# Performance work log

Hardware: AMD Instinct MI355X
Metric: run time of the kernel (lower is better)

Reference implementation:

```python
import jax, jax.numpy as jnp
import numpy as np

TAU = 2.0
EPS = 1e-5
SG_ALPHA = 4.0  # spikingjelly default Sigmoid surrogate alpha


@jax.custom_vjp
def heaviside(x):
    return (x >= 0.0).astype(x.dtype)

def _heaviside_fwd(x):
    return heaviside(x), x

def _heaviside_bwd(x, g):
    s = jax.nn.sigmoid(SG_ALPHA * x)
    return (g * SG_ALPHA * s * (1.0 - s),)

heaviside.defvjp(_heaviside_fwd, _heaviside_bwd)


def lif(x_seq, v_th):
    """Multi-step LIF, hard reset to 0, detach_reset=True. x_seq: (T, ...)."""
    def step(v, x_t):
        v = v + (x_t - v) / TAU
        s = heaviside(v - v_th)
        v = v * (1.0 - jax.lax.stop_gradient(s))  # detached hard reset
        return v, s
    _, spikes = jax.lax.scan(step, jnp.zeros_like(x_seq[0]), x_seq)
    return spikes


def bn(y, gamma, beta, mean, var):
    # y: (T, B, C, N); inference-mode BatchNorm1d over channel dim
    inv = gamma / jnp.sqrt(var + EPS)
    return y * inv[None, None, :, None] + (beta - mean * inv)[None, None, :, None]


def setup_inputs() -> dict:
    key = jax.random.key(0)
    ks = jax.random.split(key, 8)
    T, B, C, H, W = 4, 32, 256, 32, 32
    d = {
        "x": jax.random.normal(ks[0], (T, B, C, H, W), jnp.float32),
        "q_w": jax.random.normal(ks[1], (C, C), jnp.float32) * (1.0 / np.sqrt(C)),
        "q_gamma": jnp.ones((C,), jnp.float32),
        "q_beta": jnp.zeros((C,), jnp.float32),
        "q_mean": jnp.zeros((C,), jnp.float32),
        "q_var": jnp.ones((C,), jnp.float32),
        "k_w": jax.random.normal(ks[2], (C, C), jnp.float32) * (1.0 / np.sqrt(C)),
        "k_gamma": jnp.ones((C,), jnp.float32),
        "k_beta": jnp.zeros((C,), jnp.float32),
        "k_mean": jnp.zeros((C,), jnp.float32),
        "k_var": jnp.ones((C,), jnp.float32),
        "p_w": jax.random.normal(ks[3], (C, C), jnp.float32) * (1.0 / np.sqrt(C)),
        "p_b": jnp.zeros((C,), jnp.float32),
        "p_gamma": jnp.ones((C,), jnp.float32),
        "p_beta": jnp.zeros((C,), jnp.float32),
        "p_mean": jnp.zeros((C,), jnp.float32),
        "p_var": jnp.ones((C,), jnp.float32),
    }
    return d


def reference(x, q_w, q_gamma, q_beta, q_mean, q_var,
              k_w, k_gamma, k_beta, k_mean, k_var,
              p_w, p_b, p_gamma, p_beta, p_mean, p_var):
    T, B, C, H, W = x.shape
    num_heads = 8
    dh = C // num_heads
    N = H * W
    xs = x.reshape(T, B, C, N)

    # Q branch: 1x1 conv (C x C matmul) -> BN -> LIF
    q = bn(jnp.einsum('oc,tbcn->tbon', q_w, xs), q_gamma, q_beta, q_mean, q_var)
    q_spikes = lif(q, 1.0)                                # (T,B,C,N)
    q_h = q_spikes.reshape(T, B, num_heads, dh, N)

    # K branch
    k = bn(jnp.einsum('oc,tbcn->tbon', k_w, xs), k_gamma, k_beta, k_mean, k_var)
    k_spikes = lif(k, 1.0)
    k_h = k_spikes.reshape(T, B, num_heads, dh, N)

    # channel-sum pooled Q per head -> attn LIF (v_th=0.5) -> elementwise mult with K
    q_sum = jnp.sum(q_h, axis=3, keepdims=True)           # (T,B,h,1,N)
    attn = lif(q_sum, 0.5)
    x_one = attn * k_h                                    # (T,B,h,dh,N)

    # projection: 1x1 conv with bias -> BN -> LIF
    xo = x_one.reshape(T, B, C, N)
    xo = jnp.einsum('oc,tbcn->tbon', p_w, xo) + p_b[None, None, :, None]
    xo = bn(xo, p_gamma, p_beta, p_mean, p_var).reshape(T, B, C, H, W)
    x_final = lif(xo, 1.0)
    return x_final
```

## Files before the change

kernel.cpp:

```cpp
#include <hip/hip_runtime.h>
#include <cstdint>
#include <cstddef>

#define T_DIM 4
#define B_DIM 32
#define C_DIM 256
#define N_DIM 1024
#define NHEAD 8
#define DHEAD 32
#define NWRD 32

__device__ __forceinline__ float lif_step(float& v, float x, float vth) {
    v = __fadd_rn(v, __fmul_rn(__fsub_rn(x, v), 0.5f));
    const float s = (v >= vth) ? 1.0f : 0.0f;
    if (s != 0.0f) v = 0.0f;
    return s;
}

__device__ __forceinline__ void async_copy16(const float* g, float* l) {
    __builtin_amdgcn_global_load_lds(
        (const __attribute__((address_space(1))) unsigned int*)g,
        (__attribute__((address_space(3))) unsigned int*)l, 16, 0, 0);
}

#define FMA_ROW(r, av)                                \
    acc[(r)*8+0] = fmaf(av, b0.x, acc[(r)*8+0]);      \
    acc[(r)*8+1] = fmaf(av, b0.y, acc[(r)*8+1]);      \
    acc[(r)*8+2] = fmaf(av, b0.z, acc[(r)*8+2]);      \
    acc[(r)*8+3] = fmaf(av, b0.w, acc[(r)*8+3]);      \
    acc[(r)*8+4] = fmaf(av, b1.x, acc[(r)*8+4]);      \
    acc[(r)*8+5] = fmaf(av, b1.y, acc[(r)*8+5]);      \
    acc[(r)*8+6] = fmaf(av, b1.z, acc[(r)*8+6]);      \
    acc[(r)*8+7] = fmaf(av, b1.w, acc[(r)*8+7]);

#define FMA_8x8()        \
    FMA_ROW(0, a0.x)     \
    FMA_ROW(1, a0.y)     \
    FMA_ROW(2, a0.z)     \
    FMA_ROW(3, a0.w)     \
    FMA_ROW(4, a1.x)     \
    FMA_ROW(5, a1.y)     \
    FMA_ROW(6, a1.z)     \
    FMA_ROW(7, a1.w)

__global__ __launch_bounds__(256) void k_transpose(
    const float* __restrict__ qw, const float* __restrict__ kw,
    const float* __restrict__ pw, float* __restrict__ wqk_t,
    float* __restrict__ p_t)
{
    const int i = blockIdx.x * 256 + threadIdx.x;
    if (i < C_DIM * 512) {
        const int k = i >> 9, col = i & 511;
        const int h = col >> 6, j = col & 63;
        wqk_t[i] = (j < 32) ? qw[(size_t)(h * 32 + j) * C_DIM + k]
                            : kw[(size_t)(h * 32 + j - 32) * C_DIM + k];
    } else {
        const int i2 = i - C_DIM * 512;
        const int k = i2 >> 8, c = i2 & 255;
        p_t[i2] = pw[(size_t)c * C_DIM + k];
    }
}

__global__ __launch_bounds__(256, 2) void k_qk(
    const float* __restrict__ x, const float* __restrict__ wqk,
    const float* __restrict__ qg, const float* __restrict__ qbeta,
    const float* __restrict__ qmean, const float* __restrict__ qvar,
    const float* __restrict__ kg, const float* __restrict__ kbeta,
    const float* __restrict__ kmean, const float* __restrict__ kvar,
    uint32_t* __restrict__ xbits)
{
    __shared__ float w_lds[2][32 * 128];
    __shared__ float x_lds[2][32 * 128];
    __shared__ float inv_lds[128];
    __shared__ float bias_lds[128];
    __shared__ float    qsum_lds[256];
    __shared__ float    attn_lds[256];
    __shared__ uint32_t pack_lds[256];

    const int tid = threadIdx.x;
    const int hp = blockIdx.x, nt = blockIdx.y, b = blockIdx.z;
    const int n0g = nt * 128;

    const int  mg   = tid >> 4;
    const int  m0   = mg << 3;
    const int  ng   = tid & 15;
    const int  n0   = ng << 2;
    const int  hsel = mg >> 3;
    const bool is_q = ((mg & 7) < 4);

    if (tid < 128) {
        const int m = tid;
        const int hs = m >> 6, j = m & 63;
        const int h = hp * 2 + hs;
        const bool q = (j < 32);
        const float* g  = q ? qg    : kg;
        const float* be = q ? qbeta : kbeta;
        const float* me = q ? qmean : kmean;
        const float* va = q ? qvar  : kvar;
        const int ch = h * DHEAD + (q ? j : j - 32);
        const float iv = __fdiv_rn(g[ch], __fsqrt_rn(__fadd_rn(va[ch], 1e-5f)));
        inv_lds[m]  = iv;
        bias_lds[m] = __fsub_rn(be[ch], __fmul_rn(me[ch], iv));
    }

    const int skl  = tid >> 5;
    const int scol = (tid & 31) << 2;
    const float* wgp = wqk + (size_t)skl * 512 + hp * 128 + scol;

    float vstate[64];
    #pragma unroll
    for (int i = 0; i < 64; i++) vstate[i] = 0.0f;
    float v_attn = 0.0f;

    {
        const float* xgp = x + ((size_t)b * C_DIM + skl) * N_DIM + n0g + scol;
        #pragma unroll
        for (int r = 0; r < 4; r++) {
            async_copy16(wgp + (size_t)(r * 8) * 512,  &w_lds[0][r * 1024 + tid * 4]);
            async_copy16(xgp + (size_t)(r * 8) * N_DIM, &x_lds[0][r * 1024 + tid * 4]);
        }
    }

    float acc[64];
    #pragma unroll
    for (int i = 0; i < 64; i++) acc[i] = 0.0f;

    for (int g = 0; g < 32; ++g) {
        const int cur = g & 1;
        __syncthreads();
        if (g + 1 < 32) {
            const int g1 = g + 1, tt = g1 >> 3, kk = (g1 & 7) * 32;
            const float* xgp = x + ((size_t)(tt * B_DIM + b) * C_DIM + kk + skl) * N_DIM
                               + n0g + scol;
            float* wd = &w_lds[1 - cur][0];
            float* xd = &x_lds[1 - cur][0];
            #pragma unroll
            for (int r = 0; r < 4; r++) {
                async_copy16(wgp + (size_t)(kk + r * 8) * 512,  wd + r * 1024 + tid * 4);
                async_copy16(xgp + (size_t)(r * 8) * N_DIM,     xd + r * 1024 + tid * 4);
            }
        }
        {
            const float* wl = &w_lds[cur][0];
            const float* xl = &x_lds[cur][0];
            #pragma unroll 2
            for (int k = 0; k < 32; k++) {
                const float4 a0 = *(const float4*)(wl + k * 128 + m0);
                const float4 a1 = *(const float4*)(wl + k * 128 + m0 + 4);
                const float4 b0 = *(const float4*)(xl + k * 128 + n0);
                const float4 b1 = *(const float4*)(xl + k * 128 + 64 + n0);
                FMA_8x8()
            }
        }

        if ((g & 7) == 7) {
            const int t = g >> 3;
            #pragma unroll
            for (int r = 0; r < 8; r++) {
                const float iv = inv_lds[m0 + r];
                const float bs = bias_lds[m0 + r];
                #pragma unroll
                for (int j = 0; j < 8; j++) {
                    const float y = __fadd_rn(__fmul_rn(acc[r * 8 + j], iv), bs);
                    acc[r * 8 + j] = lif_step(vstate[r * 8 + j], y, 1.0f);
                }
            }
            qsum_lds[tid] = 0.0f;
            pack_lds[tid] = 0u;
            __syncthreads();
            if (is_q) {
                #pragma unroll
                for (int j = 0; j < 8; j++) {
                    const int col = (j < 4) ? (n0 + j) : (64 + n0 + (j - 4));
                    float cs = acc[j];
                    #pragma unroll
                    for (int r = 1; r < 8; r++) cs += acc[r * 8 + j];
                    atomicAdd(&qsum_lds[hsel * 128 + col], cs);
                }
            }
            __syncthreads();
            attn_lds[tid] = lif_step(v_attn, qsum_lds[tid], 0.5f);
            __syncthreads();
            if (!is_q) {
                #pragma unroll
                for (int r = 0; r < 8; r++) {
                    const int krow = ((mg & 7) - 4) * 8 + r;
                    #pragma unroll
                    for (int ci = 0; ci < 2; ci++) {
                        uint32_t nib = 0;
                        #pragma unroll
                        for (int jj = 0; jj < 4; jj++) {
                            const int col = ci * 64 + n0 + jj;
                            if (acc[r * 8 + ci * 4 + jj] != 0.0f &&
                                attn_lds[hsel * 128 + col] != 0.0f)
                                nib |= (1u << jj);
                        }
                        if (nib) {
                            const int word = ci * 2 + (ng >> 3);
                            const int shf  = (ng & 7) * 4;
                            atomicOr(&pack_lds[hsel * 128 + krow * 4 + word], nib << shf);
                        }
                    }
                }
            }
            __syncthreads();
            {
                const int hs2  = tid >> 7;
                const int rem  = tid & 127;
                const int krow = rem >> 2, word = rem & 3;
                const int ch = (hp * 2 + hs2) * DHEAD + krow;
                xbits[((size_t)(t * B_DIM + b) * C_DIM + ch) * NWRD + nt * 4 + word]
                    = pack_lds[tid];
            }
            #pragma unroll
            for (int i = 0; i < 64; i++) acc[i] = 0.0f;
        }
    }
}

__global__ __launch_bounds__(256, 2) void k_proj(
    const uint32_t* __restrict__ xbits, const float* __restrict__ pt,
    const float* __restrict__ pbias, const float* __restrict__ pg,
    const float* __restrict__ pbeta, const float* __restrict__ pmean,
    const float* __restrict__ pvar, float* __restrict__ out)
{
    __shared__ float w_lds[2][32 * 128];
    __shared__ float x_lds[2][32 * 128];
    __shared__ float inv_lds[128];
    __shared__ float bias_lds[128];
    __shared__ float pb_lds[128];

    const int tid = threadIdx.x;
    const int mt = blockIdx.x, nt = blockIdx.y, b = blockIdx.z;
    const int n0g = nt * 128;
    const int c0  = mt * 128;

    const int mg = tid >> 4, m0 = mg << 3;
    const int ng = tid & 15, n0 = ng << 2;

    if (tid < 128) {
        const int ch = c0 + tid;
        const float iv = __fdiv_rn(pg[ch], __fsqrt_rn(__fadd_rn(pvar[ch], 1e-5f)));
        inv_lds[tid]  = iv;
        bias_lds[tid] = __fsub_rn(pbeta[ch], __fmul_rn(pmean[ch], iv));
        pb_lds[tid]   = pbias[ch];
    }

    const int skl  = tid >> 5;
    const int scol = (tid & 31) << 2;
    const float* wgp = pt + (size_t)skl * 256 + c0 + scol;

    const int urow = tid >> 3, cg = tid & 7;
    const int wsel = nt * 4 + (cg >> 1);
    const int ushf = (cg & 1) * 16;

    float vstate[64];
    #pragma unroll
    for (int i = 0; i < 64; i++) vstate[i] = 0.0f;

    #define BITS_AT(G) xbits[((size_t)((G) >> 3) * B_DIM + b) * C_DIM * NWRD \
                             + (size_t)(((G) & 7) * 32 + urow) * NWRD + wsel]

    {
        const uint32_t u0 = BITS_AT(0);
        const uint32_t bits = (u0 >> ushf) & 0xffffu;
        float* xw = &x_lds[0][tid * 16];
        #pragma unroll
        for (int q4 = 0; q4 < 4; q4++) {
            float4 f;
            f.x = ((bits >> (q4 * 4 + 0)) & 1u) ? 1.0f : 0.0f;
            f.y = ((bits >> (q4 * 4 + 1)) & 1u) ? 1.0f : 0.0f;
            f.z = ((bits >> (q4 * 4 + 2)) & 1u) ? 1.0f : 0.0f;
            f.w = ((bits >> (q4 * 4 + 3)) & 1u) ? 1.0f : 0.0f;
            *(float4*)(xw + q4 * 4) = f;
        }
        #pragma unroll
        for (int r = 0; r < 4; r++)
            async_copy16(wgp + (size_t)(r * 8) * 256, &w_lds[0][r * 1024 + tid * 4]);
    }
    uint32_t u_a = BITS_AT(1);

    float acc[64];
    #pragma unroll
    for (int i = 0; i < 64; i++) acc[i] = 0.0f;

    for (int g = 0; g < 32; ++g) {
        const int cur = g & 1;
        __syncthreads();
        if (g + 1 < 32) {
            const int kk = ((g + 1) & 7) * 32;
            const uint32_t bits = (u_a >> ushf) & 0xffffu;
            float* xw = &x_lds[1 - cur][tid * 16];
            #pragma unroll
            for (int q4 = 0; q4 < 4; q4++) {
                float4 f;
                f.x = ((bits >> (q4 * 4 + 0)) & 1u) ? 1.0f : 0.0f;
                f.y = ((bits >> (q4 * 4 + 1)) & 1u) ? 1.0f : 0.0f;
                f.z = ((bits >> (q4 * 4 + 2)) & 1u) ? 1.0f : 0.0f;
                f.w = ((bits >> (q4 * 4 + 3)) & 1u) ? 1.0f : 0.0f;
                *(float4*)(xw + q4 * 4) = f;
            }
            float* wd = &w_lds[1 - cur][0];
            #pragma unroll
            for (int r = 0; r < 4; r++)
                async_copy16(wgp + (size_t)(kk + r * 8) * 256, wd + r * 1024 + tid * 4);
        }
        if (g + 2 < 32) u_a = BITS_AT(g + 2);
        {
            const float* wl = &w_lds[cur][0];
            const float* xl = &x_lds[cur][0];
            #pragma unroll 2
            for (int k = 0; k < 32; k++) {
                const float4 a0 = *(const float4*)(wl + k * 128 + m0);
                const float4 a1 = *(const float4*)(wl + k * 128 + m0 + 4);
                const float4 b0 = *(const float4*)(xl + k * 128 + n0);
                const float4 b1 = *(const float4*)(xl + k * 128 + 64 + n0);
                FMA_8x8()
            }
        }

        if ((g & 7) == 7) {
            const int t = g >> 3;
            #pragma unroll
            for (int r = 0; r < 8; r++) {
                const int ch = c0 + m0 + r;
                const float iv = inv_lds[m0 + r];
                const float bs = bias_lds[m0 + r];
                const float pb = pb_lds[m0 + r];
                float* ob = out + ((size_t)(t * B_DIM + b) * C_DIM + ch) * N_DIM + n0g;
                float oAv[4], oBv[4];
                #pragma unroll
                for (int j = 0; j < 8; j++) {
                    float y = __fadd_rn(acc[r * 8 + j], pb);
                    y = __fadd_rn(__fmul_rn(y, iv), bs);
                    const float s = lif_step(vstate[r * 8 + j], y, 1.0f);
                    if (j < 4) oAv[j] = s; else oBv[j - 4] = s;
                }
                float4 oA, oB;
                oA.x = oAv[0]; oA.y = oAv[1]; oA.z = oAv[2]; oA.w = oAv[3];
                oB.x = oBv[0]; oB.y = oBv[1]; oB.z = oBv[2]; oB.w = oBv[3];
                *(float4*)(ob + n0)      = oA;
                *(float4*)(ob + 64 + n0) = oB;
            }
            #pragma unroll
            for (int i = 0; i < 64; i++) acc[i] = 0.0f;
        }
    }
    #undef BITS_AT
}

extern "C" void kernel_launch(void* const* d_in, const int* in_sizes, int n_in,
                              void* d_out, int out_size, void* d_ws, size_t ws_size,
                              hipStream_t stream) {
    const float* x    = (const float*)d_in[0];
    const float* q_w  = (const float*)d_in[1];
    const float* q_g  = (const float*)d_in[2];
    const float* q_b  = (const float*)d_in[3];
    const float* q_m  = (const float*)d_in[4];
    const float* q_v  = (const float*)d_in[5];
    const float* k_w  = (const float*)d_in[6];
    const float* k_g  = (const float*)d_in[7];
    const float* k_b  = (const float*)d_in[8];
    const float* k_m  = (const float*)d_in[9];
    const float* k_v  = (const float*)d_in[10];
    const float* p_w  = (const float*)d_in[11];
    const float* p_b  = (const float*)d_in[12];
    const float* p_g  = (const float*)d_in[13];
    const float* p_be = (const float*)d_in[14];
    const float* p_m  = (const float*)d_in[15];
    const float* p_v  = (const float*)d_in[16];

    float*    wqk_t = (float*)d_ws;
    float*    p_t   = (float*)((char*)d_ws + 524288);
    uint32_t* xbits = (uint32_t*)((char*)d_ws + 786432);
    float*    out   = (float*)d_out;

    k_transpose<<<768, 256, 0, stream>>>(q_w, k_w, p_w, wqk_t, p_t);

    dim3 g1(NHEAD / 2, N_DIM / 128, B_DIM);
    k_qk<<<g1, 256, 0, stream>>>(x, wqk_t, q_g, q_b, q_m, q_v,
                                 k_g, k_b, k_m, k_v, xbits);

    dim3 g2(C_DIM / 128, N_DIM / 128, B_DIM);
    k_proj<<<g2, 256, 0, stream>>>(xbits, p_t, p_b, p_g, p_be, p_m, p_v, out);
}
```

Measured before the change: 832.5 us.

## Read weights via scalar loads, shrink tiles, ballot-pack spikes per wavefront

Both GEMM kernels stop staging weights in LDS. Each wavefront now owns 16 output rows, and the weights arrive through inline-asm s_load_dwordx16 scalar loads that are broadcast to all lanes, while each lane handles two columns. Per-block tiles shrink to 64 rows, register accumulators drop from 64 to 32, and launch bounds rise to 4 blocks per CU to raise occupancy. In k_qk, the LDS atomics used for the Q-sum and spike packing are replaced by a two-wave partial-sum exchange and __ballot bit packing. The trade-offs are less register-level reuse per thread, an s_waitcnt after every k-pair that stalls each scalar load, and reliance on the scalar cache for weight bandwidth.

```diff
diff --git a/kernel.cpp b/kernel.cpp
--- a/kernel.cpp
+++ b/kernel.cpp
@@ -10,6 +10,8 @@
 #define DHEAD 32
 #define NWRD 32
 
+typedef float f32x16 __attribute__((ext_vector_type(16)));
+
 __device__ __forceinline__ float lif_step(float& v, float x, float vth) {
     v = __fadd_rn(v, __fmul_rn(__fsub_rn(x, v), 0.5f));
     const float s = (v >= vth) ? 1.0f : 0.0f;
@@ -23,25 +25,33 @@
         (__attribute__((address_space(3))) unsigned int*)l, 16, 0, 0);
 }
 
-#define FMA_ROW(r, av)                                \
-    acc[(r)*8+0] = fmaf(av, b0.x, acc[(r)*8+0]);      \
-    acc[(r)*8+1] = fmaf(av, b0.y, acc[(r)*8+1]);      \
-    acc[(r)*8+2] = fmaf(av, b0.z, acc[(r)*8+2]);      \
-    acc[(r)*8+3] = fmaf(av, b0.w, acc[(r)*8+3]);      \
-    acc[(r)*8+4] = fmaf(av, b1.x, acc[(r)*8+4]);      \
-    acc[(r)*8+5] = fmaf(av, b1.y, acc[(r)*8+5]);      \
-    acc[(r)*8+6] = fmaf(av, b1.z, acc[(r)*8+6]);      \
-    acc[(r)*8+7] = fmaf(av, b1.w, acc[(r)*8+7]);
-
-#define FMA_8x8()        \
-    FMA_ROW(0, a0.x)     \
-    FMA_ROW(1, a0.y)     \
-    FMA_ROW(2, a0.z)     \
-    FMA_ROW(3, a0.w)     \
-    FMA_ROW(4, a1.x)     \
-    FMA_ROW(5, a1.y)     \
-    FMA_ROW(6, a1.z)     \
-    FMA_ROW(7, a1.w)
+#define KSTEP2(KK, WST) { \
+    f32x16 A0, A1; \
+    asm volatile("s_load_dwordx16 %0, %2, %3\n\t" \
+                 "s_load_dwordx16 %1, %2, %4\n\t" \
+                 "s_waitcnt lgkmcnt(0)" \
+                 : "=&s"(A0), "=&s"(A1) \
+                 : "s"(wb), "n"((KK) * (WST)), "n"(((KK) + 1) * (WST))); \
+    const float b0A = xl[(KK) * 128 + l]; \
+    const float b0B = xl[(KK) * 128 + 64 + l]; \
+    const float b1A = xl[(KK) * 128 + 128 + l]; \
+    const float b1B = xl[(KK) * 128 + 192 + l]; \
+    _Pragma("unroll") \
+    for (int r_ = 0; r_ < 16; ++r_) { \
+        acc[r_ * 2]     = fmaf(A0[r_], b0A, acc[r_ * 2]); \
+        acc[r_ * 2 + 1] = fmaf(A0[r_], b0B, acc[r_ * 2 + 1]); \
+    } \
+    _Pragma("unroll") \
+    for (int r_ = 0; r_ < 16; ++r_) { \
+        acc[r_ * 2]     = fmaf(A1[r_], b1A, acc[r_ * 2]); \
+        acc[r_ * 2 + 1] = fmaf(A1[r_], b1B, acc[r_ * 2 + 1]); \
+    } }
+
+#define KLOOP(WST) \
+    KSTEP2(0, WST)  KSTEP2(2, WST)  KSTEP2(4, WST)  KSTEP2(6, WST) \
+    KSTEP2(8, WST)  KSTEP2(10, WST) KSTEP2(12, WST) KSTEP2(14, WST) \
+    KSTEP2(16, WST) KSTEP2(18, WST) KSTEP2(20, WST) KSTEP2(22, WST) \
+    KSTEP2(24, WST) KSTEP2(26, WST) KSTEP2(28, WST) KSTEP2(30, WST)
 
 __global__ __launch_bounds__(256) void k_transpose(
     const float* __restrict__ qw, const float* __restrict__ kw,
@@ -61,7 +71,7 @@
     }
 }
 
-__global__ __launch_bounds__(256, 2) void k_qk(
+__global__ __launch_bounds__(256, 4) void k_qk(
     const float* __restrict__ x, const float* __restrict__ wqk,
     const float* __restrict__ qg, const float* __restrict__ qbeta,
     const float* __restrict__ qmean, const float* __restrict__ qvar,
@@ -69,176 +79,134 @@
     const float* __restrict__ kmean, const float* __restrict__ kvar,
     uint32_t* __restrict__ xbits)
 {
-    __shared__ float w_lds[2][32 * 128];
     __shared__ float x_lds[2][32 * 128];
-    __shared__ float inv_lds[128];
-    __shared__ float bias_lds[128];
-    __shared__ float    qsum_lds[256];
-    __shared__ float    attn_lds[256];
-    __shared__ uint32_t pack_lds[256];
+    __shared__ float inv_lds[64];
+    __shared__ float bias_lds[64];
+    __shared__ float qpart_lds[2][128];
 
     const int tid = threadIdx.x;
-    const int hp = blockIdx.x, nt = blockIdx.y, b = blockIdx.z;
+    const int nt = blockIdx.x, b = blockIdx.y, h = blockIdx.z;
     const int n0g = nt * 128;
-
-    const int  mg   = tid >> 4;
-    const int  m0   = mg << 3;
-    const int  ng   = tid & 15;
-    const int  n0   = ng << 2;
-    const int  hsel = mg >> 3;
-    const bool is_q = ((mg & 7) < 4);
-
-    if (tid < 128) {
-        const int m = tid;
-        const int hs = m >> 6, j = m & 63;
-        const int h = hp * 2 + hs;
+    const int l   = tid & 63;
+    const int sw  = __builtin_amdgcn_readfirstlane(tid >> 6);
+    const bool is_q = (sw < 2);
+
+    if (tid < 64) {
+        const int j = tid;
         const bool q = (j < 32);
-        const float* g  = q ? qg    : kg;
+        const float* gp = q ? qg    : kg;
         const float* be = q ? qbeta : kbeta;
         const float* me = q ? qmean : kmean;
         const float* va = q ? qvar  : kvar;
         const int ch = h * DHEAD + (q ? j : j - 32);
-        const float iv = __fdiv_rn(g[ch], __fsqrt_rn(__fadd_rn(va[ch], 1e-5f)));
-        inv_lds[m]  = iv;
-        bias_lds[m] = __fsub_rn(be[ch], __fmul_rn(me[ch], iv));
+        const float iv = __fdiv_rn(gp[ch], __fsqrt_rn(__fadd_rn(va[ch], 1e-5f)));
+        inv_lds[j]  = iv;
+        bias_lds[j] = __fsub_rn(be[ch], __fmul_rn(me[ch], iv));
     }
 
     const int skl  = tid >> 5;
     const int scol = (tid & 31) << 2;
-    const float* wgp = wqk + (size_t)skl * 512 + hp * 128 + scol;
-
-    float vstate[64];
+
+    float vstate[32];
     #pragma unroll
-    for (int i = 0; i < 64; i++) vstate[i] = 0.0f;
-    float v_attn = 0.0f;
+    for (int i = 0; i < 32; ++i) vstate[i] = 0.0f;
+    float v_attn0 = 0.0f, v_attn1 = 0.0f;
+    float acc[32];
+    #pragma unroll
+    for (int i = 0; i < 32; ++i) acc[i] = 0.0f;
 
     {
         const float* xgp = x + ((size_t)b * C_DIM + skl) * N_DIM + n0g + scol;
         #pragma unroll
-        for (int r = 0; r < 4; r++) {
-            async_copy16(wgp + (size_t)(r * 8) * 512,  &w_lds[0][r * 1024 + tid * 4]);
+        for (int r = 0; r < 4; ++r)
             async_copy16(xgp + (size_t)(r * 8) * N_DIM, &x_lds[0][r * 1024 + tid * 4]);
-        }
-    }
-
-    float acc[64];
-    #pragma unroll
-    for (int i = 0; i < 64; i++) acc[i] = 0.0f;
-
-    for (int g = 0; g < 32; ++g) {
-        const int cur = g & 1;
+    }
+
+    const size_t woff = (size_t)h * 64 + (size_t)sw * 16;
+
+    #pragma unroll 1
+    for (int gi = 0; gi < 32; ++gi) {
+        const int cur = gi & 1;
         __syncthreads();
-        if (g + 1 < 32) {
-            const int g1 = g + 1, tt = g1 >> 3, kk = (g1 & 7) * 32;
+        if (gi + 1 < 32) {
+            const int g1 = gi + 1, tt = g1 >> 3, kk = (g1 & 7) * 32;
             const float* xgp = x + ((size_t)(tt * B_DIM + b) * C_DIM + kk + skl) * N_DIM
                                + n0g + scol;
-            float* wd = &w_lds[1 - cur][0];
             float* xd = &x_lds[1 - cur][0];
             #pragma unroll
-            for (int r = 0; r < 4; r++) {
-                async_copy16(wgp + (size_t)(kk + r * 8) * 512,  wd + r * 1024 + tid * 4);
-                async_copy16(xgp + (size_t)(r * 8) * N_DIM,     xd + r * 1024 + tid * 4);
-            }
+            for (int r = 0; r < 4; ++r)
+                async_copy16(xgp + (size_t)(r * 8) * N_DIM, xd + r * 1024 + tid * 4);
         }
         {
-            const float* wl = &w_lds[cur][0];
+            const float* wb = wqk + (size_t)((gi & 7) * 32) * 512 + woff;
             const float* xl = &x_lds[cur][0];
-            #pragma unroll 2
-            for (int k = 0; k < 32; k++) {
-                const float4 a0 = *(const float4*)(wl + k * 128 + m0);
-                const float4 a1 = *(const float4*)(wl + k * 128 + m0 + 4);
-                const float4 b0 = *(const float4*)(xl + k * 128 + n0);
-                const float4 b1 = *(const float4*)(xl + k * 128 + 64 + n0);
-                FMA_8x8()
-            }
-        }
-
-        if ((g & 7) == 7) {
-            const int t = g >> 3;
-            #pragma unroll
-            for (int r = 0; r < 8; r++) {
-                const float iv = inv_lds[m0 + r];
-                const float bs = bias_lds[m0 + r];
+            KLOOP(2048)
+        }
+
+        if ((gi & 7) == 7) {
+            const int t = gi >> 3;
+            #pragma unroll
+            for (int r = 0; r < 16; ++r) {
+                const float iv = inv_lds[sw * 16 + r];
+                const float bs = bias_lds[sw * 16 + r];
+                const float y0 = __fadd_rn(__fmul_rn(acc[r * 2],     iv), bs);
+                const float y1 = __fadd_rn(__fmul_rn(acc[r * 2 + 1], iv), bs);
+                acc[r * 2]     = lif_step(vstate[r * 2],     y0, 1.0f);
+                acc[r * 2 + 1] = lif_step(vstate[r * 2 + 1], y1, 1.0f);
+            }
+            if (is_q) {
+                float pA = acc[0], pB = acc[1];
                 #pragma unroll
-                for (int j = 0; j < 8; j++) {
-                    const float y = __fadd_rn(__fmul_rn(acc[r * 8 + j], iv), bs);
-                    acc[r * 8 + j] = lif_step(vstate[r * 8 + j], y, 1.0f);
-                }
-            }
-            qsum_lds[tid] = 0.0f;
-            pack_lds[tid] = 0u;
-            __syncthreads();
-            if (is_q) {
-                #pragma unroll
-                for (int j = 0; j < 8; j++) {
-                    const int col = (j < 4) ? (n0 + j) : (64 + n0 + (j - 4));
-                    float cs = acc[j];
-                    #pragma unroll
-                    for (int r = 1; r < 8; r++) cs += acc[r * 8 + j];
-                    atomicAdd(&qsum_lds[hsel * 128 + col], cs);
-                }
-            }
-            __syncthreads();
-            attn_lds[tid] = lif_step(v_attn, qsum_lds[tid], 0.5f);
+                for (int r = 1; r < 16; ++r) { pA += acc[r * 2]; pB += acc[r * 2 + 1]; }
+                qpart_lds[sw][l]      = pA;
+                qpart_lds[sw][64 + l] = pB;
+            }
             __syncthreads();
             if (!is_q) {
+                const float qA = qpart_lds[0][l]      + qpart_lds[1][l];
+                const float qB = qpart_lds[0][64 + l] + qpart_lds[1][64 + l];
+                const float aA = lif_step(v_attn0, qA, 0.5f);
+                const float aB = lif_step(v_attn1, qB, 0.5f);
+                uint64_t k0 = 0ull, k1 = 0ull;
                 #pragma unroll
-                for (int r = 0; r < 8; r++) {
-                    const int krow = ((mg & 7) - 4) * 8 + r;
-                    #pragma unroll
-                    for (int ci = 0; ci < 2; ci++) {
-                        uint32_t nib = 0;
-                        #pragma unroll
-                        for (int jj = 0; jj < 4; jj++) {
-                            const int col = ci * 64 + n0 + jj;
-                            if (acc[r * 8 + ci * 4 + jj] != 0.0f &&
-                                attn_lds[hsel * 128 + col] != 0.0f)
-                                nib |= (1u << jj);
-                        }
-                        if (nib) {
-                            const int word = ci * 2 + (ng >> 3);
-                            const int shf  = (ng & 7) * 4;
-                            atomicOr(&pack_lds[hsel * 128 + krow * 4 + word], nib << shf);
-                        }
-                    }
+                for (int r = 0; r < 16; ++r) {
+                    const uint64_t m0 = __ballot(acc[r * 2]     != 0.0f && aA != 0.0f);
+                    const uint64_t m1 = __ballot(acc[r * 2 + 1] != 0.0f && aB != 0.0f);
+                    if (l == r) { k0 = m0; k1 = m1; }
                 }
-            }
-            __syncthreads();
-            {
-                const int hs2  = tid >> 7;
-                const int rem  = tid & 127;
-                const int krow = rem >> 2, word = rem & 3;
-                const int ch = (hp * 2 + hs2) * DHEAD + krow;
-                xbits[((size_t)(t * B_DIM + b) * C_DIM + ch) * NWRD + nt * 4 + word]
-                    = pack_lds[tid];
-            }
-            #pragma unroll
-            for (int i = 0; i < 64; i++) acc[i] = 0.0f;
-        }
-    }
-}
-
-__global__ __launch_bounds__(256, 2) void k_proj(
+                if (l < 16) {
+                    const int ch = h * DHEAD + (sw - 2) * 16 + l;
+                    uint4 v;
+                    v.x = (uint32_t)k0; v.y = (uint32_t)(k0 >> 32);
+                    v.z = (uint32_t)k1; v.w = (uint32_t)(k1 >> 32);
+                    *(uint4*)&xbits[(((size_t)t * B_DIM + b) * C_DIM + ch) * NWRD + nt * 4] = v;
+                }
+            }
+            #pragma unroll
+            for (int i = 0; i < 32; ++i) acc[i] = 0.0f;
+        }
+    }
+}
+
+__global__ __launch_bounds__(256, 4) void k_proj(
     const uint32_t* __restrict__ xbits, const float* __restrict__ pt,
     const float* __restrict__ pbias, const float* __restrict__ pg,
     const float* __restrict__ pbeta, const float* __restrict__ pmean,
     const float* __restrict__ pvar, float* __restrict__ out)
 {
-    __shared__ float w_lds[2][32 * 128];
     __shared__ float x_lds[2][32 * 128];
-    __shared__ float inv_lds[128];
-    __shared__ float bias_lds[128];
-    __shared__ float pb_lds[128];
+    __shared__ float inv_lds[64];
+    __shared__ float bias_lds[64];
+    __shared__ float pb_lds[64];
 
     const int tid = threadIdx.x;
     const int mt = blockIdx.x, nt = blockIdx.y, b = blockIdx.z;
     const int n0g = nt * 128;
-    const int c0  = mt * 128;
-
-    const int mg = tid >> 4, m0 = mg << 3;
-    const int ng = tid & 15, n0 = ng << 2;
-
-    if (tid < 128) {
+    const int c0  = mt * 64;
+    const int l   = tid & 63;
+    const int sw  = __builtin_amdgcn_readfirstlane(tid >> 6);
+
+    if (tid < 64) {
         const int ch = c0 + tid;
         const float iv = __fdiv_rn(pg[ch], __fsqrt_rn(__fadd_rn(pvar[ch], 1e-5f)));
         inv_lds[tid]  = iv;
@@ -246,17 +214,16 @@
         pb_lds[tid]   = pbias[ch];
     }
 
-    const int skl  = tid >> 5;
-    const int scol = (tid & 31) << 2;
-    const float* wgp = pt + (size_t)skl * 256 + c0 + scol;
-
     const int urow = tid >> 3, cg = tid & 7;
     const int wsel = nt * 4 + (cg >> 1);
     const int ushf = (cg & 1) * 16;
 
-    float vstate[64];
+    float vstate[32];
     #pragma unroll
-    for (int i = 0; i < 64; i++) vstate[i] = 0.0f;
+    for (int i = 0; i < 32; ++i) vstate[i] = 0.0f;
+    float acc[32];
+    #pragma unroll
+    for (int i = 0; i < 32; ++i) acc[i] = 0.0f;
 
     #define BITS_AT(G) xbits[((size_t)((G) >> 3) * B_DIM + b) * C_DIM * NWRD \
                              + (size_t)(((G) & 7) * 32 + urow) * NWRD + wsel]
@@ -266,7 +233,7 @@
         const uint32_t bits = (u0 >> ushf) & 0xffffu;
         float* xw = &x_lds[0][tid * 16];
         #pragma unroll
-        for (int q4 = 0; q4 < 4; q4++) {
+        for (int q4 = 0; q4 < 4; ++q4) {
             float4 f;
             f.x = ((bits >> (q4 * 4 + 0)) & 1u) ? 1.0f : 0.0f;
             f.y = ((bits >> (q4 * 4 + 1)) & 1u) ? 1.0f : 0.0f;
@@ -274,25 +241,20 @@
             f.w = ((bits >> (q4 * 4 + 3)) & 1u) ? 1.0f : 0.0f;
             *(float4*)(xw + q4 * 4) = f;
         }
-        #pragma unroll
-        for (int r = 0; r < 4; r++)
-            async_copy16(wgp + (size_t)(r * 8) * 256, &w_lds[0][r * 1024 + tid * 4]);
     }
     uint32_t u_a = BITS_AT(1);
 
-    float acc[64];
-    #pragma unroll
-    for (int i = 0; i < 64; i++) acc[i] = 0.0f;
-
-    for (int g = 0; g < 32; ++g) {
-        const int cur = g & 1;
+    const size_t woff = (size_t)c0 + (size_t)sw * 16;
+
+    #pragma unroll 1
+    for (int gi = 0; gi < 32; ++gi) {
+        const int cur = gi & 1;
         __syncthreads();
-        if (g + 1 < 32) {
-            const int kk = ((g + 1) & 7) * 32;
+        if (gi + 1 < 32) {
             const uint32_t bits = (u_a >> ushf) & 0xffffu;
             float* xw = &x_lds[1 - cur][tid * 16];
             #pragma unroll
-            for (int q4 = 0; q4 < 4; q4++) {
+            for (int q4 = 0; q4 < 4; ++q4) {
                 float4 f;
                 f.x = ((bits >> (q4 * 4 + 0)) & 1u) ? 1.0f : 0.0f;
                 f.y = ((bits >> (q4 * 4 + 1)) & 1u) ? 1.0f : 0.0f;
@@ -300,50 +262,34 @@
                 f.w = ((bits >> (q4 * 4 + 3)) & 1u) ? 1.0f : 0.0f;
                 *(float4*)(xw + q4 * 4) = f;
             }
-            float* wd = &w_lds[1 - cur][0];
-            #pragma unroll
-            for (int r = 0; r < 4; r++)
-                async_copy16(wgp + (size_t)(kk + r * 8) * 256, wd + r * 1024 + tid * 4);
-        }
-        if (g + 2 < 32) u_a = BITS_AT(g + 2);
+        }
+        if (gi + 2 < 32) u_a = BITS_AT(gi + 2);
         {
-            const float* wl = &w_lds[cur][0];
+            const float* wb = pt + (size_t)((gi & 7) * 32) * 256 + woff;
             const float* xl = &x_lds[cur][0];
-            #pragma unroll 2
-            for (int k = 0; k < 32; k++) {
-                const float4 a0 = *(const float4*)(wl + k * 128 + m0);
-                const float4 a1 = *(const float4*)(wl + k * 128 + m0 + 4);
-                const float4 b0 = *(const float4*)(xl + k * 128 + n0);
-                const float4 b1 = *(const float4*)(xl + k * 128 + 64 + n0);
-                FMA_8x8()
-            }
-        }
-
-        if ((g & 7) == 7) {
-            const int t = g >> 3;
-            #pragma unroll
-            for (int r = 0; r < 8; r++) {
-                const int ch = c0 + m0 + r;
-                const float iv = inv_lds[m0 + r];
-                const float bs = bias_lds[m0 + r];
-                const float pb = pb_lds[m0 + r];
-                float* ob = out + ((size_t)(t * B_DIM + b) * C_DIM + ch) * N_DIM + n0g;
-                float oAv[4], oBv[4];
-                #pragma unroll
-                for (int j = 0; j < 8; j++) {
-                    float y = __fadd_rn(acc[r * 8 + j], pb);
-                    y = __fadd_rn(__fmul_rn(y, iv), bs);
-                    const float s = lif_step(vstate[r * 8 + j], y, 1.0f);
-                    if (j < 4) oAv[j] = s; else oBv[j - 4] = s;
-                }
-                float4 oA, oB;
-                oA.x = oAv[0]; oA.y = oAv[1]; oA.z = oAv[2]; oA.w = oAv[3];
-                oB.x = oBv[0]; oB.y = oBv[1]; oB.z = oBv[2]; oB.w = oBv[3];
-                *(float4*)(ob + n0)      = oA;
-                *(float4*)(ob + 64 + n0) = oB;
-            }
-            #pragma unroll
-            for (int i = 0; i < 64; i++) acc[i] = 0.0f;
+            KLOOP(1024)
+        }
+
+        if ((gi & 7) == 7) {
+            const int t = gi >> 3;
+            #pragma unroll
+            for (int r = 0; r < 16; ++r) {
+                const int m = sw * 16 + r;
+                const float iv = inv_lds[m];
+                const float bs = bias_lds[m];
+                const float pb = pb_lds[m];
+                float y0 = __fadd_rn(acc[r * 2],     pb);
+                float y1 = __fadd_rn(acc[r * 2 + 1], pb);
+                y0 = __fadd_rn(__fmul_rn(y0, iv), bs);
+                y1 = __fadd_rn(__fmul_rn(y1, iv), bs);
+                const float s0 = lif_step(vstate[r * 2],     y0, 1.0f);
+                const float s1 = lif_step(vstate[r * 2 + 1], y1, 1.0f);
+                float* ob = out + (((size_t)t * B_DIM + b) * C_DIM + c0 + m) * N_DIM + n0g;
+                ob[l]      = s0;
+                ob[64 + l] = s1;
+            }
+            #pragma unroll
+            for (int i = 0; i < 32; ++i) acc[i] = 0.0f;
         }
     }
     #undef BITS_AT
@@ -377,10 +323,10 @@
 
     k_transpose<<<768, 256, 0, stream>>>(q_w, k_w, p_w, wqk_t, p_t);
 
-    dim3 g1(NHEAD / 2, N_DIM / 128, B_DIM);
+    dim3 g1(N_DIM / 128, B_DIM, NHEAD);
     k_qk<<<g1, 256, 0, stream>>>(x, wqk_t, q_g, q_b, q_m, q_v,
                                  k_g, k_b, k_m, k_v, xbits);
 
-    dim3 g2(C_DIM / 128, N_DIM / 128, B_DIM);
+    dim3 g2(C_DIM / 64, N_DIM / 128, B_DIM);
     k_proj<<<g2, 256, 0, stream>>>(xbits, p_t, p_b, p_g, p_be, p_m, p_v, out);
 }
```

Result: slower. 2.850 ms (+242.4%).

## Read GEMM weights directly from global memory instead of staging in LDS

Applied to the files above, without the earlier changes.

Both the QK and projection GEMM kernels stop double-buffering the weight tile in shared memory. Inside the inner k-loop each thread now loads its 8 weight values straight from global memory (or cache) as float4. This halves the LDS footprint and removes the weight async copies, and k_qk's launch bounds are raised to allow 4 blocks per CU. The cost is global or L2 latency inside the FMA loop with no prefetch, plus register pressure from 64 accumulators and 64 state values under the tighter occupancy target.

```diff
diff --git a/kernel.cpp b/kernel.cpp
--- a/kernel.cpp
+++ b/kernel.cpp
@@ -61,7 +61,7 @@
     }
 }
 
-__global__ __launch_bounds__(256, 2) void k_qk(
+__global__ __launch_bounds__(256, 4) void k_qk(
     const float* __restrict__ x, const float* __restrict__ wqk,
     const float* __restrict__ qg, const float* __restrict__ qbeta,
     const float* __restrict__ qmean, const float* __restrict__ qvar,
@@ -69,7 +69,6 @@
     const float* __restrict__ kmean, const float* __restrict__ kvar,
     uint32_t* __restrict__ xbits)
 {
-    __shared__ float w_lds[2][32 * 128];
     __shared__ float x_lds[2][32 * 128];
     __shared__ float inv_lds[128];
     __shared__ float bias_lds[128];
@@ -105,7 +104,6 @@
 
     const int skl  = tid >> 5;
     const int scol = (tid & 31) << 2;
-    const float* wgp = wqk + (size_t)skl * 512 + hp * 128 + scol;
 
     float vstate[64];
     #pragma unroll
@@ -115,10 +113,8 @@
     {
         const float* xgp = x + ((size_t)b * C_DIM + skl) * N_DIM + n0g + scol;
         #pragma unroll
-        for (int r = 0; r < 4; r++) {
-            async_copy16(wgp + (size_t)(r * 8) * 512,  &w_lds[0][r * 1024 + tid * 4]);
+        for (int r = 0; r < 4; r++)
             async_copy16(xgp + (size_t)(r * 8) * N_DIM, &x_lds[0][r * 1024 + tid * 4]);
-        }
     }
 
     float acc[64];
@@ -132,21 +128,18 @@
             const int g1 = g + 1, tt = g1 >> 3, kk = (g1 & 7) * 32;
             const float* xgp = x + ((size_t)(tt * B_DIM + b) * C_DIM + kk + skl) * N_DIM
                                + n0g + scol;
-            float* wd = &w_lds[1 - cur][0];
             float* xd = &x_lds[1 - cur][0];
             #pragma unroll
-            for (int r = 0; r < 4; r++) {
-                async_copy16(wgp + (size_t)(kk + r * 8) * 512,  wd + r * 1024 + tid * 4);
-                async_copy16(xgp + (size_t)(r * 8) * N_DIM,     xd + r * 1024 + tid * 4);
-            }
+            for (int r = 0; r < 4; r++)
+                async_copy16(xgp + (size_t)(r * 8) * N_DIM, xd + r * 1024 + tid * 4);
         }
         {
-            const float* wl = &w_lds[cur][0];
+            const float* wg = wqk + (size_t)((g & 7) * 32) * 512 + hp * 128 + m0;
             const float* xl = &x_lds[cur][0];
             #pragma unroll 2
             for (int k = 0; k < 32; k++) {
-                const float4 a0 = *(const float4*)(wl + k * 128 + m0);
-                const float4 a1 = *(const float4*)(wl + k * 128 + m0 + 4);
+                const float4 a0 = *(const float4*)(wg + (size_t)k * 512);
+                const float4 a1 = *(const float4*)(wg + (size_t)k * 512 + 4);
                 const float4 b0 = *(const float4*)(xl + k * 128 + n0);
                 const float4 b1 = *(const float4*)(xl + k * 128 + 64 + n0);
                 FMA_8x8()
@@ -224,7 +217,6 @@
     const float* __restrict__ pbeta, const float* __restrict__ pmean,
     const float* __restrict__ pvar, float* __restrict__ out)
 {
-    __shared__ float w_lds[2][32 * 128];
     __shared__ float x_lds[2][32 * 128];
     __shared__ float inv_lds[128];
     __shared__ float bias_lds[128];
@@ -245,10 +237,6 @@
         bias_lds[tid] = __fsub_rn(pbeta[ch], __fmul_rn(pmean[ch], iv));
         pb_lds[tid]   = pbias[ch];
     }
-
-    const int skl  = tid >> 5;
-    const int scol = (tid & 31) << 2;
-    const float* wgp = pt + (size_t)skl * 256 + c0 + scol;
 
     const int urow = tid >> 3, cg = tid & 7;
     const int wsel = nt * 4 + (cg >> 1);
@@ -274,9 +262,6 @@
             f.w = ((bits >> (q4 * 4 + 3)) & 1u) ? 1.0f : 0.0f;
             *(float4*)(xw + q4 * 4) = f;
         }
-        #pragma unroll
-        for (int r = 0; r < 4; r++)
-            async_copy16(wgp + (size_t)(r * 8) * 256, &w_lds[0][r * 1024 + tid * 4]);
     }
     uint32_t u_a = BITS_AT(1);
 
@@ -288,7 +273,6 @@
         const int cur = g & 1;
         __syncthreads();
         if (g + 1 < 32) {
-            const int kk = ((g + 1) & 7) * 32;
             const uint32_t bits = (u_a >> ushf) & 0xffffu;
             float* xw = &x_lds[1 - cur][tid * 16];
             #pragma unroll
@@ -300,19 +284,15 @@
                 f.w = ((bits >> (q4 * 4 + 3)) & 1u) ? 1.0f : 0.0f;
                 *(float4*)(xw + q4 * 4) = f;
             }
-            float* wd = &w_lds[1 - cur][0];
-            #pragma unroll
-            for (int r = 0; r < 4; r++)
-                async_copy16(wgp + (size_t)(kk + r * 8) * 256, wd + r * 1024 + tid * 4);
         }
         if (g + 2 < 32) u_a = BITS_AT(g + 2);
         {
-            const float* wl = &w_lds[cur][0];
+            const float* wg = pt + (size_t)((g & 7) * 32) * 256 + c0 + m0;
             const float* xl = &x_lds[cur][0];
             #pragma unroll 2
             for (int k = 0; k < 32; k++) {
-                const float4 a0 = *(const float4*)(wl + k * 128 + m0);
-                const float4 a1 = *(const float4*)(wl + k * 128 + m0 + 4);
+                const float4 a0 = *(const float4*)(wg + (size_t)k * 256);
+                const float4 a1 = *(const float4*)(wg + (size_t)k * 256 + 4);
                 const float4 b0 = *(const float4*)(xl + k * 128 + n0);
                 const float4 b1 = *(const float4*)(xl + k * 128 + 64 + n0);
                 FMA_8x8()
```

Measured after the change: 995.0 us. +19.5%, slower.

## Double threads per block and halve per-thread register tile in both GEMMs

Applied to the files above, without the earlier changes.

Both the Q/K and projection kernels move from 256 to 512 threads per block, with each thread computing an 8x4 accumulator tile instead of 8x8. Loads, LIF epilogue, spike packing and bit unpacking are re-indexed to the new thread mapping. The goal is fewer registers per thread, higher occupancy and better latency hiding. The cost is lower arithmetic intensity per LDS read, more LDS traffic per FMA, and costlier block-wide barriers.

```diff
diff --git a/kernel.cpp b/kernel.cpp
--- a/kernel.cpp
+++ b/kernel.cpp
@@ -23,25 +23,21 @@
         (__attribute__((address_space(3))) unsigned int*)l, 16, 0, 0);
 }
 
-#define FMA_ROW(r, av)                                \
-    acc[(r)*8+0] = fmaf(av, b0.x, acc[(r)*8+0]);      \
-    acc[(r)*8+1] = fmaf(av, b0.y, acc[(r)*8+1]);      \
-    acc[(r)*8+2] = fmaf(av, b0.z, acc[(r)*8+2]);      \
-    acc[(r)*8+3] = fmaf(av, b0.w, acc[(r)*8+3]);      \
-    acc[(r)*8+4] = fmaf(av, b1.x, acc[(r)*8+4]);      \
-    acc[(r)*8+5] = fmaf(av, b1.y, acc[(r)*8+5]);      \
-    acc[(r)*8+6] = fmaf(av, b1.z, acc[(r)*8+6]);      \
-    acc[(r)*8+7] = fmaf(av, b1.w, acc[(r)*8+7]);
-
-#define FMA_8x8()        \
-    FMA_ROW(0, a0.x)     \
-    FMA_ROW(1, a0.y)     \
-    FMA_ROW(2, a0.z)     \
-    FMA_ROW(3, a0.w)     \
-    FMA_ROW(4, a1.x)     \
-    FMA_ROW(5, a1.y)     \
-    FMA_ROW(6, a1.z)     \
-    FMA_ROW(7, a1.w)
+#define FMA_ROW4(r, av)                               \
+    acc[(r)*4+0] = fmaf(av, b0.x, acc[(r)*4+0]);      \
+    acc[(r)*4+1] = fmaf(av, b0.y, acc[(r)*4+1]);      \
+    acc[(r)*4+2] = fmaf(av, b0.z, acc[(r)*4+2]);      \
+    acc[(r)*4+3] = fmaf(av, b0.w, acc[(r)*4+3]);
+
+#define FMA_8x4()        \
+    FMA_ROW4(0, a0.x)    \
+    FMA_ROW4(1, a0.y)    \
+    FMA_ROW4(2, a0.z)    \
+    FMA_ROW4(3, a0.w)    \
+    FMA_ROW4(4, a1.x)    \
+    FMA_ROW4(5, a1.y)    \
+    FMA_ROW4(6, a1.z)    \
+    FMA_ROW4(7, a1.w)
 
 __global__ __launch_bounds__(256) void k_transpose(
     const float* __restrict__ qw, const float* __restrict__ kw,
@@ -61,7 +57,7 @@
     }
 }
 
-__global__ __launch_bounds__(256, 2) void k_qk(
+__global__ __launch_bounds__(512, 4) void k_qk(
     const float* __restrict__ x, const float* __restrict__ wqk,
     const float* __restrict__ qg, const float* __restrict__ qbeta,
     const float* __restrict__ qmean, const float* __restrict__ qvar,
@@ -81,9 +77,9 @@
     const int hp = blockIdx.x, nt = blockIdx.y, b = blockIdx.z;
     const int n0g = nt * 128;
 
-    const int  mg   = tid >> 4;
+    const int  mg   = tid >> 5;
     const int  m0   = mg << 3;
-    const int  ng   = tid & 15;
+    const int  ng   = tid & 31;
     const int  n0   = ng << 2;
     const int  hsel = mg >> 3;
     const bool is_q = ((mg & 7) < 4);
@@ -107,23 +103,23 @@
     const int scol = (tid & 31) << 2;
     const float* wgp = wqk + (size_t)skl * 512 + hp * 128 + scol;
 
-    float vstate[64];
+    float vstate[32];
     #pragma unroll
-    for (int i = 0; i < 64; i++) vstate[i] = 0.0f;
+    for (int i = 0; i < 32; i++) vstate[i] = 0.0f;
     float v_attn = 0.0f;
 
     {
         const float* xgp = x + ((size_t)b * C_DIM + skl) * N_DIM + n0g + scol;
         #pragma unroll
-        for (int r = 0; r < 4; r++) {
-            async_copy16(wgp + (size_t)(r * 8) * 512,  &w_lds[0][r * 1024 + tid * 4]);
-            async_copy16(xgp + (size_t)(r * 8) * N_DIM, &x_lds[0][r * 1024 + tid * 4]);
-        }
-    }
-
-    float acc[64];
+        for (int r = 0; r < 2; r++) {
+            async_copy16(wgp + (size_t)(r * 16) * 512,  &w_lds[0][r * 2048 + tid * 4]);
+            async_copy16(xgp + (size_t)(r * 16) * N_DIM, &x_lds[0][r * 2048 + tid * 4]);
+        }
+    }
+
+    float acc[32];
     #pragma unroll
-    for (int i = 0; i < 64; i++) acc[i] = 0.0f;
+    for (int i = 0; i < 32; i++) acc[i] = 0.0f;
 
     for (int g = 0; g < 32; ++g) {
         const int cur = g & 1;
@@ -135,9 +131,9 @@
             float* wd = &w_lds[1 - cur][0];
             float* xd = &x_lds[1 - cur][0];
             #pragma unroll
-            for (int r = 0; r < 4; r++) {
-                async_copy16(wgp + (size_t)(kk + r * 8) * 512,  wd + r * 1024 + tid * 4);
-                async_copy16(xgp + (size_t)(r * 8) * N_DIM,     xd + r * 1024 + tid * 4);
+            for (int r = 0; r < 2; r++) {
+                async_copy16(wgp + (size_t)(kk + r * 16) * 512,  wd + r * 2048 + tid * 4);
+                async_copy16(xgp + (size_t)(r * 16) * N_DIM,     xd + r * 2048 + tid * 4);
             }
         }
         {
@@ -148,8 +144,7 @@
                 const float4 a0 = *(const float4*)(wl + k * 128 + m0);
                 const float4 a1 = *(const float4*)(wl + k * 128 + m0 + 4);
                 const float4 b0 = *(const float4*)(xl + k * 128 + n0);
-                const float4 b1 = *(const float4*)(xl + k * 128 + 64 + n0);
-                FMA_8x8()
+                FMA_8x4()
             }
         }
 
@@ -160,51 +155,46 @@
                 const float iv = inv_lds[m0 + r];
                 const float bs = bias_lds[m0 + r];
                 #pragma unroll
-                for (int j = 0; j < 8; j++) {
-                    const float y = __fadd_rn(__fmul_rn(acc[r * 8 + j], iv), bs);
-                    acc[r * 8 + j] = lif_step(vstate[r * 8 + j], y, 1.0f);
+                for (int j = 0; j < 4; j++) {
+                    const float y = __fadd_rn(__fmul_rn(acc[r * 4 + j], iv), bs);
+                    acc[r * 4 + j] = lif_step(vstate[r * 4 + j], y, 1.0f);
                 }
             }
-            qsum_lds[tid] = 0.0f;
-            pack_lds[tid] = 0u;
+            if (tid < 256) { qsum_lds[tid] = 0.0f; pack_lds[tid] = 0u; }
             __syncthreads();
             if (is_q) {
                 #pragma unroll
-                for (int j = 0; j < 8; j++) {
-                    const int col = (j < 4) ? (n0 + j) : (64 + n0 + (j - 4));
+                for (int j = 0; j < 4; j++) {
+                    const int col = n0 + j;
                     float cs = acc[j];
                     #pragma unroll
-                    for (int r = 1; r < 8; r++) cs += acc[r * 8 + j];
+                    for (int r = 1; r < 8; r++) cs += acc[r * 4 + j];
                     atomicAdd(&qsum_lds[hsel * 128 + col], cs);
                 }
             }
             __syncthreads();
-            attn_lds[tid] = lif_step(v_attn, qsum_lds[tid], 0.5f);
+            if (tid < 256) attn_lds[tid] = lif_step(v_attn, qsum_lds[tid], 0.5f);
             __syncthreads();
             if (!is_q) {
                 #pragma unroll
                 for (int r = 0; r < 8; r++) {
                     const int krow = ((mg & 7) - 4) * 8 + r;
+                    uint32_t nib = 0;
                     #pragma unroll
-                    for (int ci = 0; ci < 2; ci++) {
-                        uint32_t nib = 0;
-                        #pragma unroll
-                        for (int jj = 0; jj < 4; jj++) {
-                            const int col = ci * 64 + n0 + jj;
-                            if (acc[r * 8 + ci * 4 + jj] != 0.0f &&
-                                attn_lds[hsel * 128 + col] != 0.0f)
-                                nib |= (1u << jj);
-                        }
-                        if (nib) {
-                            const int word = ci * 2 + (ng >> 3);
-                            const int shf  = (ng & 7) * 4;
-                            atomicOr(&pack_lds[hsel * 128 + krow * 4 + word], nib << shf);
-                        }
+                    for (int jj = 0; jj < 4; jj++) {
+                        if (acc[r * 4 + jj] != 0.0f &&
+                            attn_lds[hsel * 128 + n0 + jj] != 0.0f)
+                            nib |= (1u << jj);
+                    }
+                    if (nib) {
+                        const int word = ng >> 3;
+                        const int shf  = (ng & 7) * 4;
+                        atomicOr(&pack_lds[hsel * 128 + krow * 4 + word], nib << shf);
                     }
                 }
             }
             __syncthreads();
-            {
+            if (tid < 256) {
                 const int hs2  = tid >> 7;
                 const int rem  = tid & 127;
                 const int krow = rem >> 2, word = rem & 3;
@@ -213,12 +203,12 @@
                     = pack_lds[tid];
             }
             #pragma unroll
-            for (int i = 0; i < 64; i++) acc[i] = 0.0f;
-        }
-    }
-}
-
-__global__ __launch_bounds__(256, 2) void k_proj(
+            for (int i = 0; i < 32; i++) acc[i] = 0.0f;
+        }
+    }
+}
+
+__global__ __launch_bounds__(512, 4) void k_proj(
     const uint32_t* __restrict__ xbits, const float* __restrict__ pt,
     const float* __restrict__ pbias, const float* __restrict__ pg,
     const float* __restrict__ pbeta, const float* __restrict__ pmean,
@@ -235,8 +225,8 @@
     const int n0g = nt * 128;
     const int c0  = mt * 128;
 
-    const int mg = tid >> 4, m0 = mg << 3;
-    const int ng = tid & 15, n0 = ng << 2;
+    const int mg = tid >> 5, m0 = mg << 3;
+    const int ng = tid & 31, n0 = ng << 2;
 
     if (tid < 128) {
         const int ch = c0 + tid;
@@ -250,60 +240,64 @@
     const int scol = (tid & 31) << 2;
     const float* wgp = pt + (size_t)skl * 256 + c0 + scol;
 
-    const int urow = tid >> 3, cg = tid & 7;
-    const int wsel = nt * 4 + (cg >> 1);
-    const int ushf = (cg & 1) * 16;
-
-    float vstate[64];
+    const int urow = tid >> 4, cg = tid & 15;
+    const int wsel = nt * 4 + (cg >> 2);
+    const int ushf = (cg & 3) * 8;
+
+    float vstate[32];
     #pragma unroll
-    for (int i = 0; i < 64; i++) vstate[i] = 0.0f;
+    for (int i = 0; i < 32; i++) vstate[i] = 0.0f;
 
     #define BITS_AT(G) xbits[((size_t)((G) >> 3) * B_DIM + b) * C_DIM * NWRD \
                              + (size_t)(((G) & 7) * 32 + urow) * NWRD + wsel]
 
     {
         const uint32_t u0 = BITS_AT(0);
-        const uint32_t bits = (u0 >> ushf) & 0xffffu;
-        float* xw = &x_lds[0][tid * 16];
+        const uint32_t bits = (u0 >> ushf) & 0xffu;
+        float* xw = &x_lds[0][urow * 128 + cg * 8];
+        float4 f0, f1;
+        f0.x = ((bits >> 0) & 1u) ? 1.0f : 0.0f;
+        f0.y = ((bits >> 1) & 1u) ? 1.0f : 0.0f;
+        f0.z = ((bits >> 2) & 1u) ? 1.0f : 0.0f;
+        f0.w = ((bits >> 3) & 1u) ? 1.0f : 0.0f;
+        f1.x = ((bits >> 4) & 1u) ? 1.0f : 0.0f;
+        f1.y = ((bits >> 5) & 1u) ? 1.0f : 0.0f;
+        f1.z = ((bits >> 6) & 1u) ? 1.0f : 0.0f;
+        f1.w = ((bits >> 7) & 1u) ? 1.0f : 0.0f;
+        *(float4*)(xw)     = f0;
+        *(float4*)(xw + 4) = f1;
         #pragma unroll
-        for (int q4 = 0; q4 < 4; q4++) {
-            float4 f;
-            f.x = ((bits >> (q4 * 4 + 0)) & 1u) ? 1.0f : 0.0f;
-            f.y = ((bits >> (q4 * 4 + 1)) & 1u) ? 1.0f : 0.0f;
-            f.z = ((bits >> (q4 * 4 + 2)) & 1u) ? 1.0f : 0.0f;
-            f.w = ((bits >> (q4 * 4 + 3)) & 1u) ? 1.0f : 0.0f;
-            *(float4*)(xw + q4 * 4) = f;
-        }
-        #pragma unroll
-        for (int r = 0; r < 4; r++)
-            async_copy16(wgp + (size_t)(r * 8) * 256, &w_lds[0][r * 1024 + tid * 4]);
+        for (int r = 0; r < 2; r++)
+            async_copy16(wgp + (size_t)(r * 16) * 256, &w_lds[0][r * 2048 + tid * 4]);
     }
     uint32_t u_a = BITS_AT(1);
 
-    float acc[64];
+    float acc[32];
     #pragma unroll
-    for (int i = 0; i < 64; i++) acc[i] = 0.0f;
+    for (int i = 0; i < 32; i++) acc[i] = 0.0f;
 
     for (int g = 0; g < 32; ++g) {
         const int cur = g & 1;
         __syncthreads();
         if (g + 1 < 32) {
             const int kk = ((g + 1) & 7) * 32;
-            const uint32_t bits = (u_a >> ushf) & 0xffffu;
-            float* xw = &x_lds[1 - cur][tid * 16];
-            #pragma unroll
-            for (int q4 = 0; q4 < 4; q4++) {
-                float4 f;
-                f.x = ((bits >> (q4 * 4 + 0)) & 1u) ? 1.0f : 0.0f;
-                f.y = ((bits >> (q4 * 4 + 1)) & 1u) ? 1.0f : 0.0f;
-                f.z = ((bits >> (q4 * 4 + 2)) & 1u) ? 1.0f : 0.0f;
-                f.w = ((bits >> (q4 * 4 + 3)) & 1u) ? 1.0f : 0.0f;
-                *(float4*)(xw + q4 * 4) = f;
-            }
+            const uint32_t bits = (u_a >> ushf) & 0xffu;
+            float* xw = &x_lds[1 - cur][urow * 128 + cg * 8];
+            float4 f0, f1;
+            f0.x = ((bits >> 0) & 1u) ? 1.0f : 0.0f;
+            f0.y = ((bits >> 1) & 1u) ? 1.0f : 0.0f;
+            f0.z = ((bits >> 2) & 1u) ? 1.0f : 0.0f;
+            f0.w = ((bits >> 3) & 1u) ? 1.0f : 0.0f;
+            f1.x = ((bits >> 4) & 1u) ? 1.0f : 0.0f;
+            f1.y = ((bits >> 5) & 1u) ? 1.0f : 0.0f;
+            f1.z = ((bits >> 6) & 1u) ? 1.0f : 0.0f;
+            f1.w = ((bits >> 7) & 1u) ? 1.0f : 0.0f;
+            *(float4*)(xw)     = f0;
+            *(float4*)(xw + 4) = f1;
             float* wd = &w_lds[1 - cur][0];
             #pragma unroll
-            for (int r = 0; r < 4; r++)
-                async_copy16(wgp + (size_t)(kk + r * 8) * 256, wd + r * 1024 + tid * 4);
+            for (int r = 0; r < 2; r++)
+                async_copy16(wgp + (size_t)(kk + r * 16) * 256, wd + r * 2048 + tid * 4);
         }
         if (g + 2 < 32) u_a = BITS_AT(g + 2);
         {
@@ -314,8 +308,7 @@
                 const float4 a0 = *(const float4*)(wl + k * 128 + m0);
                 const float4 a1 = *(const float4*)(wl + k * 128 + m0 + 4);
                 const float4 b0 = *(const float4*)(xl + k * 128 + n0);
-                const float4 b1 = *(const float4*)(xl + k * 128 + 64 + n0);
-                FMA_8x8()
+                FMA_8x4()
             }
         }
 
@@ -328,22 +321,19 @@
                 const float bs = bias_lds[m0 + r];
                 const float pb = pb_lds[m0 + r];
                 float* ob = out + ((size_t)(t * B_DIM + b) * C_DIM + ch) * N_DIM + n0g;
-                float oAv[4], oBv[4];
+                float ov[4];
                 #pragma unroll
-                for (int j = 0; j < 8; j++) {
-                    float y = __fadd_rn(acc[r * 8 + j], pb);
+                for (int j = 0; j < 4; j++) {
+                    float y = __fadd_rn(acc[r * 4 + j], pb);
                     y = __fadd_rn(__fmul_rn(y, iv), bs);
-                    const float s = lif_step(vstate[r * 8 + j], y, 1.0f);
-                    if (j < 4) oAv[j] = s; else oBv[j - 4] = s;
+                    ov[j] = lif_step(vstate[r * 4 + j], y, 1.0f);
                 }
-                float4 oA, oB;
-                oA.x = oAv[0]; oA.y = oAv[1]; oA.z = oAv[2]; oA.w = oAv[3];
-                oB.x = oBv[0]; oB.y = oBv[1]; oB.z = oBv[2]; oB.w = oBv[3];
-                *(float4*)(ob + n0)      = oA;
-                *(float4*)(ob + 64 + n0) = oB;
-            }
-            #pragma unroll
-            for (int i = 0; i < 64; i++) acc[i] = 0.0f;
+                float4 o4;
+                o4.x = ov[0]; o4.y = ov[1]; o4.z = ov[2]; o4.w = ov[3];
+                *(float4*)(ob + n0) = o4;
+            }
+            #pragma unroll
+            for (int i = 0; i < 32; i++) acc[i] = 0.0f;
         }
     }
     #undef BITS_AT
@@ -378,9 +368,9 @@
     k_transpose<<<768, 256, 0, stream>>>(q_w, k_w, p_w, wqk_t, p_t);
 
     dim3 g1(NHEAD / 2, N_DIM / 128, B_DIM);
-    k_qk<<<g1, 256, 0, stream>>>(x, wqk_t, q_g, q_b, q_m, q_v,
+    k_qk<<<g1, 512, 0, stream>>>(x, wqk_t, q_g, q_b, q_m, q_v,
                                  k_g, k_b, k_m, k_v, xbits);
 
     dim3 g2(C_DIM / 128, N_DIM / 128, B_DIM);
-    k_proj<<<g2, 256, 0, stream>>>(xbits, p_t, p_b, p_g, p_be, p_m, p_v, out);
-}
+    k_proj<<<g2, 512, 0, stream>>>(xbits, p_t, p_b, p_g, p_be, p_m, p_v, out);
+}
```

New measurement: 846.9 us. About the same (+1.7%).
